# Performance work log

Hardware: AMD Instinct MI355X
Metric: run time of the kernel (lower is better)

## Reference

```python
import jax, jax.numpy as jnp
import numpy as np

ENC_IN = 64
D_MODEL = 512
B, T = 256, 256


def setup_inputs() -> dict:
    key = jax.random.key(0)
    ks = jax.random.split(key, 16)
    d = D_MODEL
    std = 1.0 / np.sqrt(d)
    def w(k, shape):
        return jax.random.normal(k, shape, dtype=jnp.float32) * std
    return {
        'x': jax.random.normal(ks[0], (B, T, ENC_IN), dtype=jnp.float32),
        'Wa': w(ks[1], (d, 2 * d)),
        'Ua': w(ks[2], (d, 2 * d)),
        'ba': jnp.zeros((2 * d,), jnp.float32),
        'Wna': w(ks[3], (d, d)),
        'Una': w(ks[4], (d, d)),
        'bna': jnp.zeros((d,), jnp.float32),
        'WAttn': w(ks[5], (d, d)),
        'UAttn': w(ks[6], (d, d)),
        'VAttn': w(ks[7], (d, d)),
        'Wma': w(ks[8], (d, d)),
        'Uma': w(ks[9], (d, d)),
        'bma': jax.random.normal(ks[10], (d,), dtype=jnp.float32),  # bias init torch.randn, dim==1 so not re-initialized
        'Wm': w(ks[11], (ENC_IN, 2 * d)),
        'Um': w(ks[12], (d, 2 * d)),
        'bm': jnp.zeros((2 * d,), jnp.float32),
        'Whm': w(ks[13], (ENC_IN, d)),
        'Uhm': w(ks[14], (d, d)),
        'bhm': jnp.zeros((d,), jnp.float32),
    }


def reference(x, Wa, Ua, ba, Wna, Una, bna, WAttn, UAttn, VAttn,
              Wma, Uma, bma, Wm, Um, bm, Whm, Uhm, bhm):
    Bsz = x.shape[0]
    H = Wna.shape[0]

    def step(carry, x_t):
        h, N, h_pp = carry           # h = h_{t-1}, h_pp = h_{t-2}
        d_t = h - h_pp               # 0 at t=0, h_0 at t=1, diff otherwise
        gates_A = d_t @ Wa + N @ Ua + ba
        z_A = jax.nn.sigmoid(gates_A[:, :H])
        r_A = jax.nn.sigmoid(gates_A[:, H:])
        hat_N = jnp.tanh(d_t @ Wna + (N * r_A) @ Una + bna)
        N_new = (1.0 - z_A) * N + z_A * hat_N
        score = jnp.tanh(h @ WAttn + N_new @ UAttn) @ VAttn
        alpha = jax.nn.softmax(score, axis=1)
        Omega = alpha * N_new
        m = jnp.tanh(Omega @ Wma + h @ Uma + bma)
        gates_M = x_t @ Wm + m @ Um + bm
        z_M = jax.nn.sigmoid(gates_M[:, :H])
        r_M = jax.nn.sigmoid(gates_M[:, H:])
        hat_h = jnp.tanh(x_t @ Whm + (m * r_M) @ Uhm + bhm)
        h_new = (1.0 - z_M) * h + z_M * hat_h
        return (h_new, N_new, h), h_new

    h0 = jnp.zeros((Bsz, H), x.dtype)
    init = (h0, h0, h0)
    (h_T, N_T, _), hs = jax.lax.scan(step, init, jnp.swapaxes(x, 0, 1))  # hs: [T,B,H]
    hidden_seq = jnp.swapaxes(hs, 0, 1)  # [B,T,H]
    return hidden_seq, (h_T, N_T)
```

## Files before the change

### kernel.cpp

```cpp
#include <hip/hip_runtime.h>

static constexpr int Bsz  = 256;
static constexpr int Tseq = 256;
static constexpr int Hd   = 512;
static constexpr int Ein  = 64;
static constexpr int NBLK = 256;
static constexpr int NTHR = 512;

typedef __attribute__((ext_vector_type(8))) short bf16x8;
typedef __attribute__((ext_vector_type(4))) float f32x4;
typedef unsigned long long u64;

__device__ __forceinline__ float sigm(float x) { return 1.f / (1.f + expf(-x)); }
__device__ __forceinline__ short f2bf(float f) {
  union { float f; unsigned u; } v; v.f = f;
  unsigned r = v.u + 0x7FFFu + ((v.u >> 16) & 1u);
  return (short)(r >> 16);
}
__device__ __forceinline__ float bf2f(short s) {
  union { float f; unsigned u; } v; v.u = ((unsigned)(unsigned short)s) << 16; return v.f;
}

__device__ __forceinline__ void llc_ld4(f32x4& d, const float* p) {
  asm volatile("global_load_dwordx4 %0, %1, off sc0 sc1" : "=v"(d) : "v"(p));
}
__device__ __forceinline__ void llc_st1(float* p, float v) {
  asm volatile("global_store_dword %0, %1, off sc0 sc1" :: "v"(p), "v"(v) : "memory");
}
__device__ __forceinline__ void vwait() {
  asm volatile("s_waitcnt vmcnt(0)" ::: "memory");
  __builtin_amdgcn_sched_barrier(0);
}

struct KP {
  const float *x, *ba, *bna, *bma, *bm, *bhm;
  const short *Wh[13], *Wl[13];
  float *Hbuf, *Nst, *NrA, *s1, *score, *mbuf, *mrM, *out;
  unsigned* cnt;
};

__global__ __launch_bounds__(256)
void prepack(const float* __restrict__ W, short* __restrict__ Whi,
             short* __restrict__ Wlo, int N)
{
  __shared__ float lds[32][257];
  const int tid = threadIdx.x;
  const int k0 = blockIdx.y * 32;
  const int n0 = blockIdx.x * 256;
  #pragma unroll
  for (int i = 0; i < 8; ++i) {
    const int flat = (i * 256 + tid) * 4;
    const int r = flat >> 8, c = flat & 255;
    const float4 v = *(const float4*)(W + (size_t)(k0 + r) * N + n0 + c);
    lds[r][c] = v.x; lds[r][c + 1] = v.y; lds[r][c + 2] = v.z; lds[r][c + 3] = v.w;
  }
  __syncthreads();
  const int lane = tid & 63, wv = tid >> 6;
  const int kr = (lane >> 4) * 8;
  const int cc = lane & 15;
  for (int nt = wv; nt < 16; nt += 4) {
    const int ntg = (n0 >> 4) + nt;
    const size_t off = ((size_t)((k0 >> 5) * (N >> 4) + ntg) * 64 + lane) * 8;
    bf16x8 vh, vl;
    #pragma unroll
    for (int j = 0; j < 8; ++j) {
      const float v = lds[kr + j][nt * 16 + cc];
      const short hb = f2bf(v);
      vh[j] = hb; vl[j] = f2bf(v - bf2f(hb));
    }
    *(bf16x8*)(Whi + off) = vh;
    *(bf16x8*)(Wlo + off) = vl;
  }
}

__device__ __forceinline__ int aoff(int task) {
  return (task << 3) ^ (((task >> 4) & 7) << 3);
}
__device__ __forceinline__ void task_write(int task, f32x4 u0, f32x4 u1,
                                           short* hi, short* lo) {
  const int o = aoff(task);
  bf16x8 vh, vl;
  #pragma unroll
  for (int j = 0; j < 4; ++j) {
    const short h0 = f2bf(u0[j]); vh[j]     = h0; vl[j]     = f2bf(u0[j] - bf2f(h0));
    const short h1 = f2bf(u1[j]); vh[j + 4] = h1; vl[j + 4] = f2bf(u1[j] - bf2f(h1));
  }
  *(bf16x8*)(hi + o) = vh;
  *(bf16x8*)(lo + o) = vl;
}

__device__ __forceinline__ void stageSlice(const float* src, short* hi, short* lo,
                                           int wid, int lane) {
  const int ra = wid, rb = wid + 8;
  const float* pa = src + (ra << 9) + (lane << 3);
  const float* pb = src + (rb << 9) + (lane << 3);
  f32x4 a0, a1, b0, b1;
  llc_ld4(a0, pa); llc_ld4(a1, pa + 4);
  llc_ld4(b0, pb); llc_ld4(b1, pb + 4);
  vwait();
  const int tbase = ((lane >> 2) << 6) | ((lane & 3) << 4);
  task_write(tbase | ra, a0, a1, hi, lo);
  task_write(tbase | rb, b0, b1, hi, lo);
}

__device__ __forceinline__ void mm(const short* Ah, const short* Al,
                                   const short* __restrict__ Wh,
                                   const short* __restrict__ Wl,
                                   int ntN, int ntg, int kc0, int kc1,
                                   int lane, f32x4& acc)
{
  for (int kc = kc0; kc < kc1; ++kc) {
    const int ao = aoff((kc << 6) | lane);
    const bf16x8 ah = *(const bf16x8*)(Ah + ao);
    const bf16x8 al = *(const bf16x8*)(Al + ao);
    const size_t o = ((size_t)((kc * ntN + ntg) << 6 | lane)) << 3;
    const bf16x8 bh = *(const bf16x8*)(Wh + o);
    const bf16x8 bl = *(const bf16x8*)(Wl + o);
    acc = __builtin_amdgcn_mfma_f32_16x16x32_bf16(ah, bh, acc, 0, 0, 0);
    acc = __builtin_amdgcn_mfma_f32_16x16x32_bf16(al, bh, acc, 0, 0, 0);
    acc = __builtin_amdgcn_mfma_f32_16x16x32_bf16(ah, bl, acc, 0, 0, 0);
  }
}

__device__ __forceinline__ void gbar(unsigned* cnt, int stripe, unsigned& ph) {
  asm volatile("s_waitcnt vmcnt(0)" ::: "memory");
  __syncthreads();
  ++ph;
  if (threadIdx.x == 0) {
    __hip_atomic_fetch_add(&cnt[stripe << 4], 1u, __ATOMIC_RELAXED,
                           __HIP_MEMORY_SCOPE_AGENT);
    const unsigned tgt = ph * 16u;
    while (__hip_atomic_load(&cnt[stripe << 4], __ATOMIC_RELAXED,
                             __HIP_MEMORY_SCOPE_AGENT) < tgt)
      __builtin_amdgcn_s_sleep(4);
  }
  __syncthreads();
}

__global__ __launch_bounds__(NTHR, 1)
void dtgru(KP P)
{
  __shared__ short sAh[8192], sAl[8192];
  __shared__ short sBh[8192], sBl[8192];
  __shared__ short sCh[8192], sCl[8192];
  __shared__ short sDh[8192], sDl[8192];
  __shared__ short sXh[1024], sXl[1024];
  __shared__ float red[2048];
  const int tid = threadIdx.x, lane = tid & 63, wid = tid >> 6;
  const int bid = blockIdx.x;
  const int g = bid & 15;
  const int stripe = bid >> 4;
  const int r0 = stripe << 4;
  const int nt = wid & 1;
  const int q  = wid >> 1;
  const int mat  = (wid >> 1) & 1;
  const int half = wid >> 2;
  const int ntb = (g << 1) | nt;
  const int col5 = (g << 5) | (nt << 4) | (lane & 15);
  const int rb = r0 + ((lane >> 4) << 2);
  unsigned ph = 0;
  float Nreg[4] = {0,0,0,0}, hreg[4] = {0,0,0,0};
  float zAreg[4] = {0,0,0,0}, zMreg[4] = {0,0,0,0}, mreg[4] = {0,0,0,0};
  const float b_az = P.ba[col5],  b_ar = P.ba[col5 + 512];
  const float b_na = P.bna[col5], b_ma = P.bma[col5];
  const float b_mz = P.bm[col5],  b_mr = P.bm[col5 + 512];
  const float b_hm = P.bhm[col5];

  for (int i = tid; i < 2048; i += NTHR) {
    ((u64*)sBh)[i] = 0; ((u64*)sBl)[i] = 0;
    ((u64*)sDh)[i] = 0; ((u64*)sDl)[i] = 0;
  }
  __syncthreads();

  #pragma clang loop unroll(disable)
  for (int t = 0; t < Tseq; ++t) {
    {
      const int tbase = ((lane >> 2) << 6) | ((lane & 3) << 4);
      const int ra = wid, rbw = wid + 8;
      const float* Hr = P.Hbuf + (r0 << 9);
      const float* pa = Hr + (ra << 9) + (lane << 3);
      const float* pb = Hr + (rbw << 9) + (lane << 3);
      f32x4 u0, u1, v0, v1, x0 = {0,0,0,0}, x1 = {0,0,0,0};
      llc_ld4(u0, pa); llc_ld4(u1, pa + 4);
      llc_ld4(v0, pb); llc_ld4(v1, pb + 4);
      if (tid < 128) {
        const float* px = P.x + ((size_t)(r0 + (tid >> 3)) * Tseq + t) * Ein
                        + ((tid & 7) << 3);
        x0 = *(const f32x4*)px; x1 = *(const f32x4*)(px + 4);
      }
      vwait();
      {
        const int ta = tbase | ra;
        const int o = aoff(ta);
        const bf16x8 dh = *(const bf16x8*)(sDh + o), dlo = *(const bf16x8*)(sDl + o);
        f32x4 d0, d1;
        #pragma unroll
        for (int j = 0; j < 4; ++j) {
          d0[j] = u0[j] - (bf2f(dh[j])     + bf2f(dlo[j]));
          d1[j] = u1[j] - (bf2f(dh[j + 4]) + bf2f(dlo[j + 4]));
        }
        task_write(ta, d0, d1, sAh, sAl);
        task_write(ta, u0, u1, sDh, sDl);
      }
      {
        const int tb = tbase | rbw;
        const int o = aoff(tb);
        const bf16x8 dh = *(const bf16x8*)(sDh + o), dlo = *(const bf16x8*)(sDl + o);
        f32x4 d0, d1;
        #pragma unroll
        for (int j = 0; j < 4; ++j) {
          d0[j] = v0[j] - (bf2f(dh[j])     + bf2f(dlo[j]));
          d1[j] = v1[j] - (bf2f(dh[j + 4]) + bf2f(dlo[j + 4]));
        }
        task_write(tb, d0, d1, sAh, sAl);
        task_write(tb, v0, v1, sDh, sDl);
      }
      if (tid < 128) {
        const int tx = (((tid & 7) >> 2) << 6) | (tid >> 3) | ((tid & 3) << 4);
        task_write(tx, x0, x1, sXh, sXl);
      }
    }
    __syncthreads();
    {
      f32x4 acc = {0,0,0,0};
      const int ntg = (half ? 32 : 0) | ((g << 1) | nt);
      if (!mat) mm(sAh, sAl, P.Wh[0], P.Wl[0], 64, ntg, 0, 16, lane, acc);
      else      mm(sBh, sBl, P.Wh[1], P.Wl[1], 64, ntg, 0, 16, lane, acc);
      if (mat) *(f32x4*)&red[(((half << 1) | nt) << 8) | (lane << 2)] = acc;
      __syncthreads();
      if (!mat) acc += *(f32x4*)&red[(((half << 1) | nt) << 8) | (lane << 2)];
      __syncthreads();
      if (!mat && half) *(f32x4*)&red[(nt << 8) | (lane << 2)] = acc;
      __syncthreads();
      if (!mat && !half) {
        const f32x4 ar = *(const f32x4*)&red[(nt << 8) | (lane << 2)];
        #pragma unroll
        for (int i = 0; i < 4; ++i) {
          zAreg[i] = sigm(acc[i] + b_az);
          const float rA = sigm(ar[i] + b_ar);
          llc_st1(&P.NrA[((rb + i) << 9) | col5], Nreg[i] * rA);
        }
      }
    }
    gbar(P.cnt, stripe, ph);

    stageSlice(P.NrA + (r0 << 9), sBh, sBl, wid, lane);
    __syncthreads();
    {
      f32x4 acc = {0,0,0,0};
      const int kc0 = (q & 1) << 3;
      if (!(q >> 1)) mm(sAh, sAl, P.Wh[2], P.Wl[2], 32, ntb, kc0, kc0 + 8, lane, acc);
      else           mm(sBh, sBl, P.Wh[3], P.Wl[3], 32, ntb, kc0, kc0 + 8, lane, acc);
      if (q) *(f32x4*)&red[((((q - 1) << 1) | nt) << 8) | (lane << 2)] = acc;
      __syncthreads();
      if (!q) {
        #pragma unroll
        for (int j = 0; j < 3; ++j) acc += *(f32x4*)&red[(((j << 1) | nt) << 8) | (lane << 2)];
        #pragma unroll
        for (int i = 0; i < 4; ++i) {
          const float hn = tanhf(acc[i] + b_na);
          const float Nn = (1.f - zAreg[i]) * Nreg[i] + zAreg[i] * hn;
          Nreg[i] = Nn;
          llc_st1(&P.Nst[((rb + i) << 9) | col5], Nn);
        }
      }
    }
    gbar(P.cnt, stripe, ph);

    stageSlice(P.Nst + (r0 << 9), sBh, sBl, wid, lane);
    __syncthreads();
    {
      f32x4 acc = {0,0,0,0};
      const int kc0 = (q & 1) << 3;
      if (!(q >> 1)) mm(sDh, sDl, P.Wh[4], P.Wl[4], 32, ntb, kc0, kc0 + 8, lane, acc);
      else           mm(sBh, sBl, P.Wh[5], P.Wl[5], 32, ntb, kc0, kc0 + 8, lane, acc);
      if (q) *(f32x4*)&red[((((q - 1) << 1) | nt) << 8) | (lane << 2)] = acc;
      __syncthreads();
      if (!q) {
        #pragma unroll
        for (int j = 0; j < 3; ++j) acc += *(f32x4*)&red[(((j << 1) | nt) << 8) | (lane << 2)];
        #pragma unroll
        for (int i = 0; i < 4; ++i)
          llc_st1(&P.s1[((rb + i) << 9) | col5], tanhf(acc[i]));
      }
    }
    gbar(P.cnt, stripe, ph);

    stageSlice(P.s1 + (r0 << 9), sCh, sCl, wid, lane);
    __syncthreads();
    {
      f32x4 acc = {0,0,0,0};
      mm(sCh, sCl, P.Wh[6], P.Wl[6], 32, ntb, q << 2, (q << 2) + 4, lane, acc);
      if (q) *(f32x4*)&red[((((q - 1) << 1) | nt) << 8) | (lane << 2)] = acc;
      __syncthreads();
      if (!q) {
        #pragma unroll
        for (int j = 0; j < 3; ++j) acc += *(f32x4*)&red[(((j << 1) | nt) << 8) | (lane << 2)];
        #pragma unroll
        for (int i = 0; i < 4; ++i)
          llc_st1(&P.score[((rb + i) << 9) | col5], acc[i]);
      }
    }
    gbar(P.cnt, stripe, ph);

    {
      const int lr0 = wid << 1;
      f32x4 s00, s01, s10, s11;
      llc_ld4(s00, P.score + ((r0 + lr0) << 9) + (lane << 3));
      llc_ld4(s01, P.score + ((r0 + lr0) << 9) + (lane << 3) + 4);
      llc_ld4(s10, P.score + ((r0 + lr0 + 1) << 9) + (lane << 3));
      llc_ld4(s11, P.score + ((r0 + lr0 + 1) << 9) + (lane << 3) + 4);
      vwait();
      #pragma unroll
      for (int rr = 0; rr < 2; ++rr) {
        const int lr = lr0 | rr;
        const f32x4 v0 = rr ? s10 : s00, v1 = rr ? s11 : s01;
        float mx = v0[0];
        #pragma unroll
        for (int j = 1; j < 4; ++j) mx = fmaxf(mx, v0[j]);
        #pragma unroll
        for (int j = 0; j < 4; ++j) mx = fmaxf(mx, v1[j]);
        #pragma unroll
        for (int d = 1; d < 64; d <<= 1) mx = fmaxf(mx, __shfl_xor(mx, d));
        float e[8];
        #pragma unroll
        for (int j = 0; j < 4; ++j) { e[j] = expf(v0[j] - mx); e[j + 4] = expf(v1[j] - mx); }
        float sm = ((e[0] + e[1]) + (e[2] + e[3])) + ((e[4] + e[5]) + (e[6] + e[7]));
        #pragma unroll
        for (int d = 1; d < 64; d <<= 1) sm += __shfl_xor(sm, d);
        const float inv = 1.f / sm;
        const int o = aoff(((lane >> 2) << 6) | lr | ((lane & 3) << 4));
        const bf16x8 nh = *(const bf16x8*)(sBh + o), nl = *(const bf16x8*)(sBl + o);
        bf16x8 vh, vl;
        #pragma unroll
        for (int j = 0; j < 8; ++j) {
          const float om = e[j] * inv * (bf2f(nh[j]) + bf2f(nl[j]));
          const short hb = f2bf(om);
          vh[j] = hb; vl[j] = f2bf(om - bf2f(hb));
        }
        *(bf16x8*)(sCh + o) = vh;
        *(bf16x8*)(sCl + o) = vl;
      }
    }
    __syncthreads();
    {
      f32x4 acc = {0,0,0,0};
      const int kc0 = (q & 1) << 3;
      if (!(q >> 1)) mm(sCh, sCl, P.Wh[7], P.Wl[7], 32, ntb, kc0, kc0 + 8, lane, acc);
      else           mm(sDh, sDl, P.Wh[8], P.Wl[8], 32, ntb, kc0, kc0 + 8, lane, acc);
      if (q) *(f32x4*)&red[((((q - 1) << 1) | nt) << 8) | (lane << 2)] = acc;
      __syncthreads();
      if (!q) {
        #pragma unroll
        for (int j = 0; j < 3; ++j) acc += *(f32x4*)&red[(((j << 1) | nt) << 8) | (lane << 2)];
        #pragma unroll
        for (int i = 0; i < 4; ++i) {
          const float m = tanhf(acc[i] + b_ma);
          mreg[i] = m;
          llc_st1(&P.mbuf[((rb + i) << 9) | col5], m);
        }
      }
    }
    gbar(P.cnt, stripe, ph);

    stageSlice(P.mbuf + (r0 << 9), sAh, sAl, wid, lane);
    __syncthreads();
    {
      f32x4 acc = {0,0,0,0};
      const int ntg = (half ? 32 : 0) | ((g << 1) | nt);
      if (!mat) { mm(sXh, sXl, P.Wh[9],  P.Wl[9],  64, ntg, 0, 2, lane, acc);
                  mm(sAh, sAl, P.Wh[10], P.Wl[10], 64, ntg, 0, 7, lane, acc); }
      else      { mm(sAh, sAl, P.Wh[10], P.Wl[10], 64, ntg, 7, 16, lane, acc); }
      if (mat) *(f32x4*)&red[(((half << 1) | nt) << 8) | (lane << 2)] = acc;
      __syncthreads();
      if (!mat) acc += *(f32x4*)&red[(((half << 1) | nt) << 8) | (lane << 2)];
      __syncthreads();
      if (!mat && half) *(f32x4*)&red[(nt << 8) | (lane << 2)] = acc;
      __syncthreads();
      if (!mat && !half) {
        const f32x4 ar = *(const f32x4*)&red[(nt << 8) | (lane << 2)];
        #pragma unroll
        for (int i = 0; i < 4; ++i) {
          zMreg[i] = sigm(acc[i] + b_mz);
          const float rM = sigm(ar[i] + b_mr);
          llc_st1(&P.mrM[((rb + i) << 9) | col5], mreg[i] * rM);
        }
      }
    }
    gbar(P.cnt, stripe, ph);

    stageSlice(P.mrM + (r0 << 9), sCh, sCl, wid, lane);
    __syncthreads();
    {
      f32x4 acc = {0,0,0,0};
      if (q == 0)      { mm(sXh, sXl, P.Wh[11], P.Wl[11], 32, ntb, 0, 2, lane, acc);
                         mm(sCh, sCl, P.Wh[12], P.Wl[12], 32, ntb, 0, 2, lane, acc); }
      else if (q == 1)   mm(sCh, sCl, P.Wh[12], P.Wl[12], 32, ntb, 2, 7, lane, acc);
      else if (q == 2)   mm(sCh, sCl, P.Wh[12], P.Wl[12], 32, ntb, 7, 12, lane, acc);
      else               mm(sCh, sCl, P.Wh[12], P.Wl[12], 32, ntb, 12, 16, lane, acc);
      if (q) *(f32x4*)&red[((((q - 1) << 1) | nt) << 8) | (lane << 2)] = acc;
      __syncthreads();
      if (!q) {
        #pragma unroll
        for (int j = 0; j < 3; ++j) acc += *(f32x4*)&red[(((j << 1) | nt) << 8) | (lane << 2)];
        #pragma unroll
        for (int i = 0; i < 4; ++i) {
          const float hh = tanhf(acc[i] + b_hm);
          const float hn = (1.f - zMreg[i]) * hreg[i] + zMreg[i] * hh;
          hreg[i] = hn;
          llc_st1(&P.Hbuf[((rb + i) << 9) | col5], hn);
          P.out[((((size_t)(rb + i)) << 8 | t) << 9) | col5] = hn;
        }
      }
    }
    gbar(P.cnt, stripe, ph);
  }
}

__global__ __launch_bounds__(256)
void initk(float* hbuf, unsigned* cnt) {
  const int i = blockIdx.x * 256 + threadIdx.x;
  hbuf[i] = 0.f;
  if (blockIdx.x == 0) cnt[threadIdx.x] = 0u;
}

__global__ __launch_bounds__(256)
void finalize(const float* __restrict__ hT, const float* __restrict__ nT,
              float* __restrict__ oh, float* __restrict__ on) {
  const int i = blockIdx.x * 256 + threadIdx.x;
  f32x4 a, b;
  asm volatile("global_load_dword %0, %1, off sc0 sc1" : "=v"(a[0]) : "v"(&hT[i]));
  asm volatile("global_load_dword %0, %1, off sc0 sc1" : "=v"(b[0]) : "v"(&nT[i]));
  vwait();
  oh[i] = a[0]; on[i] = b[0];
}

extern "C" void kernel_launch(void* const* d_in, const int* in_sizes, int n_in,
                              void* d_out, int out_size, void* d_ws, size_t ws_size,
                              hipStream_t stream)
{
  (void)in_sizes; (void)n_in; (void)out_size; (void)ws_size;

  unsigned* cnt = (unsigned*)d_ws;
  float* w = (float*)d_ws + 256;
  const int S = Bsz * Hd;

  KP P{};
  P.x   = (const float*)d_in[0];
  P.ba  = (const float*)d_in[3];
  P.bna = (const float*)d_in[6];
  P.bma = (const float*)d_in[12];
  P.bm  = (const float*)d_in[15];
  P.bhm = (const float*)d_in[18];
  P.Hbuf = w;          P.Nst = w + S;      P.NrA = w + 2 * S;
  P.s1   = w + 3 * S;  P.score = w + 4 * S;
  P.mbuf = w + 5 * S;  P.mrM = w + 6 * S;
  P.out = (float*)d_out;
  P.cnt = cnt;
  float* out_hT = P.out + (size_t)Bsz * Tseq * Hd;
  float* out_NT = out_hT + S;

  short* wpk = (short*)(w + 7 * S);
  const int widx[13] = {1, 2, 4, 5, 7, 8, 9, 10, 11, 13, 14, 16, 17};
  const int wK[13]   = {512, 512, 512, 512, 512, 512, 512, 512, 512, 64, 512, 64, 512};
  const int wN[13]   = {1024, 1024, 512, 512, 512, 512, 512, 512, 512, 1024, 1024, 512, 512};
  {
    size_t off = 0;
    for (int i = 0; i < 13; ++i) {
      const size_t sz = (size_t)wK[i] * wN[i];
      P.Wh[i] = wpk + off; off += sz;
      P.Wl[i] = wpk + off; off += sz;
    }
  }
  for (int i = 0; i < 13; ++i) {
    dim3 gg(wN[i] / 256, wK[i] / 32);
    prepack<<<gg, 256, 0, stream>>>((const float*)d_in[widx[i]],
                                    (short*)P.Wh[i], (short*)P.Wl[i], wN[i]);
  }

  initk<<<S / 256, 256, 0, stream>>>(P.Hbuf, cnt);

  dtgru<<<NBLK, NTHR, 0, stream>>>(P);

  finalize<<<S / 256, 256, 0, stream>>>(P.Hbuf, P.Nst, out_hT, out_NT);
}
```

Before: 22.57 ms.

## Share staged activation rows between paired blocks on the same XCC via L2

```diff
diff --git a/kernel.cpp b/kernel.cpp
--- a/kernel.cpp
+++ b/kernel.cpp
@@ -27,6 +27,12 @@
 __device__ __forceinline__ void llc_st1(float* p, float v) {
   asm volatile("global_store_dword %0, %1, off sc0 sc1" :: "v"(p), "v"(v) : "memory");
 }
+__device__ __forceinline__ void l2_ld4(f32x4& d, const float* p) {
+  asm volatile("global_load_dwordx4 %0, %1, off sc0" : "=v"(d) : "v"(p));
+}
+__device__ __forceinline__ void l2_st4(float* p, f32x4 v) {
+  asm volatile("global_store_dwordx4 %0, %1, off sc0" :: "v"(p), "v"(v) : "memory");
+}
 __device__ __forceinline__ void vwait() {
   asm volatile("s_waitcnt vmcnt(0)" ::: "memory");
   __builtin_amdgcn_sched_barrier(0);
@@ -36,6 +42,7 @@
   const float *x, *ba, *bna, *bma, *bm, *bhm;
   const short *Wh[13], *Wl[13];
   float *Hbuf, *Nst, *NrA, *s1, *score, *mbuf, *mrM, *out;
+  float* pairbuf;
   unsigned* cnt;
 };
 
@@ -89,18 +96,50 @@
   *(bf16x8*)(lo + o) = vl;
 }
 
-__device__ __forceinline__ void stageSlice(const float* src, short* hi, short* lo,
-                                           int wid, int lane) {
-  const int ra = wid, rb = wid + 8;
-  const float* pa = src + (ra << 9) + (lane << 3);
-  const float* pb = src + (rb << 9) + (lane << 3);
-  f32x4 a0, a1, b0, b1;
-  llc_ld4(a0, pa); llc_ld4(a1, pa + 4);
-  llc_ld4(b0, pb); llc_ld4(b1, pb + 4);
-  vwait();
-  const int tbase = ((lane >> 2) << 6) | ((lane & 3) << 4);
-  task_write(tbase | ra, a0, a1, hi, lo);
-  task_write(tbase | rb, b0, b1, hi, lo);
+struct PairCtx {
+  float* mybuf; const float* pbuf;
+  unsigned *myflag, *pflag;
+  unsigned pfc;
+  int relay, myhalf;
+};
+
+__device__ __forceinline__ void pairWait(PairCtx& C, int tid) {
+  asm volatile("s_waitcnt vmcnt(0)" ::: "memory");
+  __syncthreads();
+  C.pfc++;
+  if (tid == 0) {
+    __hip_atomic_fetch_add(C.myflag, 1u, __ATOMIC_RELAXED, __HIP_MEMORY_SCOPE_AGENT);
+    while (__hip_atomic_load(C.pflag, __ATOMIC_RELAXED, __HIP_MEMORY_SCOPE_AGENT) < C.pfc)
+      __builtin_amdgcn_s_sleep(2);
+  }
+  __syncthreads();
+}
+
+__device__ __forceinline__ void pairStage(const float* src, short* hi, short* lo,
+                                          PairCtx& C, int wid, int lane, int tid) {
+  const int tb = ((lane >> 2) << 6) | ((lane & 3) << 4);
+  if (C.relay) {
+    const int mrow = (C.myhalf << 3) | wid;
+    const float* p = src + (mrow << 9) + (lane << 3);
+    f32x4 a0, a1; llc_ld4(a0, p); llc_ld4(a1, p + 4); vwait();
+    task_write(tb | mrow, a0, a1, hi, lo);
+    float* q = C.mybuf + (wid << 9) + (lane << 3);
+    l2_st4(q, a0); l2_st4(q + 4, a1);
+    pairWait(C, tid);
+    const int prow = ((C.myhalf ^ 1) << 3) | wid;
+    const float* r = C.pbuf + (wid << 9) + (lane << 3);
+    f32x4 b0, b1; l2_ld4(b0, r); l2_ld4(b1, r + 4); vwait();
+    task_write(tb | prow, b0, b1, hi, lo);
+  } else {
+    const float* pa = src + (wid << 9) + (lane << 3);
+    const float* pb = src + ((wid + 8) << 9) + (lane << 3);
+    f32x4 a0, a1, b0, b1;
+    llc_ld4(a0, pa); llc_ld4(a1, pa + 4);
+    llc_ld4(b0, pb); llc_ld4(b1, pb + 4);
+    vwait();
+    task_write(tb | wid, a0, a1, hi, lo);
+    task_write(tb | (wid + 8), b0, b1, hi, lo);
+  }
 }
 
 __device__ __forceinline__ void mm(const short* Ah, const short* Al,
@@ -146,6 +185,7 @@
   __shared__ short sDh[8192], sDl[8192];
   __shared__ short sXh[1024], sXl[1024];
   __shared__ float red[2048];
+  __shared__ int s_relay;
   const int tid = threadIdx.x, lane = tid & 63, wid = tid >> 6;
   const int bid = blockIdx.x;
   const int g = bid & 15;
@@ -166,32 +206,47 @@
   const float b_mz = P.bm[col5],  b_mr = P.bm[col5 + 512];
   const float b_hm = P.bhm[col5];
 
+  const int member = g >> 3;
+  const int pairid = (stripe << 3) | (g & 7);
+  unsigned* pbase = P.cnt + 256 + (pairid << 4);
+  PairCtx C;
+  C.myflag = pbase + (member << 2);
+  C.pflag  = pbase + ((member ^ 1) << 2);
+  C.mybuf  = P.pairbuf + ((size_t)((pairid << 1) | member) << 12);
+  C.pbuf   = P.pairbuf + ((size_t)((pairid << 1) | (member ^ 1)) << 12);
+  C.pfc = 0; C.myhalf = member;
+  unsigned my_xcc = 0xFFFFu;
+  asm volatile("s_getreg_b32 %0, hwreg(HW_REG_XCC_ID)" : "=s"(my_xcc));
+  if (tid == 0)
+    __hip_atomic_store(pbase + 8 + (member << 1), my_xcc + 1u,
+                       __ATOMIC_RELAXED, __HIP_MEMORY_SCOPE_AGENT);
+
   for (int i = tid; i < 2048; i += NTHR) {
     ((u64*)sBh)[i] = 0; ((u64*)sBl)[i] = 0;
     ((u64*)sDh)[i] = 0; ((u64*)sDl)[i] = 0;
   }
+  gbar(P.cnt, stripe, ph);
+  if (tid == 0) {
+    const unsigned px = __hip_atomic_load(pbase + 8 + ((member ^ 1) << 1),
+                                          __ATOMIC_RELAXED, __HIP_MEMORY_SCOPE_AGENT);
+    s_relay = (my_xcc < 8u && px == my_xcc + 1u) ? 1 : 0;
+  }
   __syncthreads();
+  C.relay = s_relay;
 
   #pragma clang loop unroll(disable)
   for (int t = 0; t < Tseq; ++t) {
     {
-      const int tbase = ((lane >> 2) << 6) | ((lane & 3) << 4);
-      const int ra = wid, rbw = wid + 8;
-      const float* Hr = P.Hbuf + (r0 << 9);
-      const float* pa = Hr + (ra << 9) + (lane << 3);
-      const float* pb = Hr + (rbw << 9) + (lane << 3);
-      f32x4 u0, u1, v0, v1, x0 = {0,0,0,0}, x1 = {0,0,0,0};
-      llc_ld4(u0, pa); llc_ld4(u1, pa + 4);
-      llc_ld4(v0, pb); llc_ld4(v1, pb + 4);
+      f32x4 x0 = {0,0,0,0}, x1 = {0,0,0,0};
       if (tid < 128) {
         const float* px = P.x + ((size_t)(r0 + (tid >> 3)) * Tseq + t) * Ein
                         + ((tid & 7) << 3);
         x0 = *(const f32x4*)px; x1 = *(const f32x4*)(px + 4);
       }
-      vwait();
-      {
-        const int ta = tbase | ra;
-        const int o = aoff(ta);
+      const int tb = ((lane >> 2) << 6) | ((lane & 3) << 4);
+      const float* Hr = P.Hbuf + (r0 << 9);
+      auto p1w = [&](int task, f32x4 u0, f32x4 u1) {
+        const int o = aoff(task);
         const bf16x8 dh = *(const bf16x8*)(sDh + o), dlo = *(const bf16x8*)(sDl + o);
         f32x4 d0, d1;
         #pragma unroll
@@ -199,21 +254,30 @@
           d0[j] = u0[j] - (bf2f(dh[j])     + bf2f(dlo[j]));
           d1[j] = u1[j] - (bf2f(dh[j + 4]) + bf2f(dlo[j + 4]));
         }
-        task_write(ta, d0, d1, sAh, sAl);
-        task_write(ta, u0, u1, sDh, sDl);
-      }
-      {
-        const int tb = tbase | rbw;
-        const int o = aoff(tb);
-        const bf16x8 dh = *(const bf16x8*)(sDh + o), dlo = *(const bf16x8*)(sDl + o);
-        f32x4 d0, d1;
-        #pragma unroll
-        for (int j = 0; j < 4; ++j) {
-          d0[j] = v0[j] - (bf2f(dh[j])     + bf2f(dlo[j]));
-          d1[j] = v1[j] - (bf2f(dh[j + 4]) + bf2f(dlo[j + 4]));
-        }
-        task_write(tb, d0, d1, sAh, sAl);
-        task_write(tb, v0, v1, sDh, sDl);
+        task_write(task, d0, d1, sAh, sAl);
+        task_write(task, u0, u1, sDh, sDl);
+      };
+      if (C.relay) {
+        const int mrow = (C.myhalf << 3) | wid;
+        const float* p = Hr + (mrow << 9) + (lane << 3);
+        f32x4 a0, a1; llc_ld4(a0, p); llc_ld4(a1, p + 4); vwait();
+        p1w(tb | mrow, a0, a1);
+        float* q2 = C.mybuf + (wid << 9) + (lane << 3);
+        l2_st4(q2, a0); l2_st4(q2 + 4, a1);
+        pairWait(C, tid);
+        const int prow = ((C.myhalf ^ 1) << 3) | wid;
+        const float* pr = C.pbuf + (wid << 9) + (lane << 3);
+        f32x4 b0, b1; l2_ld4(b0, pr); l2_ld4(b1, pr + 4); vwait();
+        p1w(tb | prow, b0, b1);
+      } else {
+        const float* pa = Hr + (wid << 9) + (lane << 3);
+        const float* pb = Hr + ((wid + 8) << 9) + (lane << 3);
+        f32x4 a0, a1, b0, b1;
+        llc_ld4(a0, pa); llc_ld4(a1, pa + 4);
+        llc_ld4(b0, pb); llc_ld4(b1, pb + 4);
+        vwait();
+        p1w(tb | wid, a0, a1);
+        p1w(tb | (wid + 8), b0, b1);
       }
       if (tid < 128) {
         const int tx = (((tid & 7) >> 2) << 6) | (tid >> 3) | ((tid & 3) << 4);
@@ -244,7 +308,7 @@
     }
     gbar(P.cnt, stripe, ph);
 
-    stageSlice(P.NrA + (r0 << 9), sBh, sBl, wid, lane);
+    pairStage(P.NrA + (r0 << 9), sBh, sBl, C, wid, lane, tid);
     __syncthreads();
     {
       f32x4 acc = {0,0,0,0};
@@ -267,7 +331,7 @@
     }
     gbar(P.cnt, stripe, ph);
 
-    stageSlice(P.Nst + (r0 << 9), sBh, sBl, wid, lane);
+    pairStage(P.Nst + (r0 << 9), sBh, sBl, C, wid, lane, tid);
     __syncthreads();
     {
       f32x4 acc = {0,0,0,0};
@@ -286,7 +350,7 @@
     }
     gbar(P.cnt, stripe, ph);
 
-    stageSlice(P.s1 + (r0 << 9), sCh, sCl, wid, lane);
+    pairStage(P.s1 + (r0 << 9), sCh, sCl, C, wid, lane, tid);
     __syncthreads();
     {
       f32x4 acc = {0,0,0,0};
@@ -304,17 +368,41 @@
     gbar(P.cnt, stripe, ph);
 
     {
+      auto srow = [&](int r) -> float* {
+        return (r < 8) ? ((float*)sAh + (r << 9)) : ((float*)sAl + ((r & 7) << 9));
+      };
+      const float* src = P.score + (r0 << 9);
+      if (C.relay) {
+        const int mrow = (C.myhalf << 3) | wid;
+        const float* p = src + (mrow << 9) + (lane << 3);
+        f32x4 a0, a1; llc_ld4(a0, p); llc_ld4(a1, p + 4); vwait();
+        { float* d = srow(mrow) + (lane << 3); *(f32x4*)d = a0; *(f32x4*)(d + 4) = a1; }
+        float* q2 = C.mybuf + (wid << 9) + (lane << 3);
+        l2_st4(q2, a0); l2_st4(q2 + 4, a1);
+        pairWait(C, tid);
+        const int prow = ((C.myhalf ^ 1) << 3) | wid;
+        const float* pr = C.pbuf + (wid << 9) + (lane << 3);
+        f32x4 b0, b1; l2_ld4(b0, pr); l2_ld4(b1, pr + 4); vwait();
+        { float* d = srow(prow) + (lane << 3); *(f32x4*)d = b0; *(f32x4*)(d + 4) = b1; }
+      } else {
+        f32x4 a0, a1, b0, b1;
+        llc_ld4(a0, src + (wid << 9) + (lane << 3));
+        llc_ld4(a1, src + (wid << 9) + (lane << 3) + 4);
+        llc_ld4(b0, src + ((wid + 8) << 9) + (lane << 3));
+        llc_ld4(b1, src + ((wid + 8) << 9) + (lane << 3) + 4);
+        vwait();
+        { float* d = srow(wid) + (lane << 3);     *(f32x4*)d = a0; *(f32x4*)(d + 4) = a1; }
+        { float* d = srow(wid + 8) + (lane << 3); *(f32x4*)d = b0; *(f32x4*)(d + 4) = b1; }
+      }
+      __syncthreads();
       const int lr0 = wid << 1;
-      f32x4 s00, s01, s10, s11;
-      llc_ld4(s00, P.score + ((r0 + lr0) << 9) + (lane << 3));
-      llc_ld4(s01, P.score + ((r0 + lr0) << 9) + (lane << 3) + 4);
-      llc_ld4(s10, P.score + ((r0 + lr0 + 1) << 9) + (lane << 3));
-      llc_ld4(s11, P.score + ((r0 + lr0 + 1) << 9) + (lane << 3) + 4);
-      vwait();
       #pragma unroll
       for (int rr = 0; rr < 2; ++rr) {
         const int lr = lr0 | rr;
-        const f32x4 v0 = rr ? s10 : s00, v1 = rr ? s11 : s01;
+        const float* sp = ((lr < 8) ? ((const float*)sAh + (lr << 9))
+                                    : ((const float*)sAl + ((lr & 7) << 9))) + (lane << 3);
+        const f32x4 v0 = *(const f32x4*)sp;
+        const f32x4 v1 = *(const f32x4*)(sp + 4);
         float mx = v0[0];
         #pragma unroll
         for (int j = 1; j < 4; ++j) mx = fmaxf(mx, v0[j]);
@@ -363,7 +451,7 @@
     }
     gbar(P.cnt, stripe, ph);
 
-    stageSlice(P.mbuf + (r0 << 9), sAh, sAl, wid, lane);
+    pairStage(P.mbuf + (r0 << 9), sAh, sAl, C, wid, lane, tid);
     __syncthreads();
     {
       f32x4 acc = {0,0,0,0};
@@ -389,7 +477,7 @@
     }
     gbar(P.cnt, stripe, ph);
 
-    stageSlice(P.mrM + (r0 << 9), sCh, sCl, wid, lane);
+    pairStage(P.mrM + (r0 << 9), sCh, sCl, C, wid, lane, tid);
     __syncthreads();
     {
       f32x4 acc = {0,0,0,0};
@@ -421,7 +509,7 @@
 void initk(float* hbuf, unsigned* cnt) {
   const int i = blockIdx.x * 256 + threadIdx.x;
   hbuf[i] = 0.f;
-  if (blockIdx.x == 0) cnt[threadIdx.x] = 0u;
+  if (blockIdx.x < 16) cnt[blockIdx.x * 256 + threadIdx.x] = 0u;
 }
 
 __global__ __launch_bounds__(256)
@@ -442,7 +530,7 @@
   (void)in_sizes; (void)n_in; (void)out_size; (void)ws_size;
 
   unsigned* cnt = (unsigned*)d_ws;
-  float* w = (float*)d_ws + 256;
+  float* w = (float*)d_ws + 4096;
   const int S = Bsz * Hd;
 
   KP P{};
@@ -464,14 +552,14 @@
   const int widx[13] = {1, 2, 4, 5, 7, 8, 9, 10, 11, 13, 14, 16, 17};
   const int wK[13]   = {512, 512, 512, 512, 512, 512, 512, 512, 512, 64, 512, 64, 512};
   const int wN[13]   = {1024, 1024, 512, 512, 512, 512, 512, 512, 512, 1024, 1024, 512, 512};
-  {
-    size_t off = 0;
-    for (int i = 0; i < 13; ++i) {
-      const size_t sz = (size_t)wK[i] * wN[i];
-      P.Wh[i] = wpk + off; off += sz;
-      P.Wl[i] = wpk + off; off += sz;
-    }
-  }
+  size_t woff = 0;
+  for (int i = 0; i < 13; ++i) {
+    const size_t sz = (size_t)wK[i] * wN[i];
+    P.Wh[i] = wpk + woff; woff += sz;
+    P.Wl[i] = wpk + woff; woff += sz;
+  }
+  P.pairbuf = (float*)(wpk + woff);
+
   for (int i = 0; i < 13; ++i) {
     dim3 gg(wN[i] / 256, wK[i] / 32);
     prepack<<<gg, 256, 0, stream>>>((const float*)d_in[widx[i]],
```

Result: faster. 21.72 ms (-3.8%).
